# Performance work log

Measured on AMD Instinct MI355X. Metric: run time of the kernel, lower is better.

The kernel has to match this reference:

```python
import jax, jax.numpy as jnp
import numpy as np
from jax import lax

EQN = 10  # equations per pixel in FlowLayer


def build_a(h, w):
    """Dense constraint basis a[num, EQN, 4*num] (<=2 nonzeros per row), as in FlowLayer.__init__."""
    num = h * w
    a = np.zeros((num, EQN, 4 * num), np.float32)
    for i in range(num):
        right = (i + 1) % w != 0 and i + 1 < num
        down = i + w < num
        if right:
            a[i, 0, 2 * num + i] = 1.0; a[i, 0, i + 1] = -1.0
            a[i, 2, 2 * num + i] = 1.0; a[i, 2, 2 * num + i + 1] = -1.0
            a[i, 4, i] = 1.0;           a[i, 4, i + 1] = -1.0
            a[i, 6, 3 * num + i] = 1.0; a[i, 6, 3 * num + i + 1] = -1.0
            a[i, 8, num + i] = 1.0;     a[i, 8, num + i + 1] = -1.0
        if down:
            a[i, 1, 3 * num + i] = 1.0; a[i, 1, num + i + w] = -1.0
            a[i, 3, 3 * num + i] = 1.0; a[i, 3, 3 * num + i + w] = -1.0
            a[i, 5, num + i] = 1.0;     a[i, 5, num + i + w] = -1.0
            a[i, 7, 2 * num + i] = 1.0; a[i, 7, 2 * num + i + w] = -1.0
            a[i, 9, i] = 1.0;           a[i, 9, i + w] = -1.0
    last = num - 1  # anchor equations for the last pixel
    a[last, 0, 2 * num + last] = 1.0
    a[last, 1, 3 * num + last] = 1.0
    a[last, 2, 2 * num + last] = 1.0
    a[last, 3, 3 * num + last] = 1.0
    a[last, 4, last] = 1.0
    a[last, 5, num + last] = 1.0
    a[last, 6, 3 * num + last] = 1.0
    a[last, 7, 2 * num + last] = 1.0
    a[last, 8, num + last] = 1.0
    a[last, 9, last] = 1.0
    return a


def conv2d(x, w, b):
    y = lax.conv_general_dilated(x, w, (1, 1), 'SAME',
                                 dimension_numbers=('NCHW', 'OIHW', 'NCHW'))
    return y + b[None, :, None, None]


def setup_inputs() -> dict:
    key = jax.random.key(0)
    N, C, H, W, GR = 4, 64, 16, 16, 4
    ks = jax.random.split(key, 12)
    s3, s1 = 0.04, 0.1  # ~1/sqrt(fan_in) scales
    inp = {
        'x': jax.random.normal(ks[0], (N, C, H, W), jnp.float32),
        'grad_w1': jax.random.normal(ks[1], (C, C, 3, 3), jnp.float32) * s3,
        'grad_b1': jnp.zeros((C,), jnp.float32),
        'grad_w2': jax.random.normal(ks[2], (EQN * GR, C, 3, 3), jnp.float32) * s3,
        'grad_b2': jnp.zeros((EQN * GR,), jnp.float32),
        'att_w1': jax.random.normal(ks[3], (C, C, 3, 3), jnp.float32) * s3,
        'att_b1': jnp.zeros((C,), jnp.float32),
        'att_w2': jax.random.normal(ks[4], (EQN * GR, C, 3, 3), jnp.float32) * s3,
        'att_b2': jnp.zeros((EQN * GR,), jnp.float32),
        'se_w1': jax.random.normal(ks[5], (C // 2, C, 1, 1), jnp.float32) * s1,
        'se_b1': jnp.zeros((C // 2,), jnp.float32),
        'se_w2': jax.random.normal(ks[6], (4 * GR, C // 2, 1, 1), jnp.float32) * s1,
        'se_b2': jnp.zeros((4 * GR,), jnp.float32),
        'gn_w': jnp.ones((4 * GR,), jnp.float32),
        'gn_b': jnp.zeros((4 * GR,), jnp.float32),
        'post_w': jax.random.normal(ks[7], (128, 4 * GR, 3, 3), jnp.float32) * s1,
        'post_b': jnp.zeros((128,), jnp.float32),
    }
    return inp


def reference(x, grad_w1, grad_b1, grad_w2, grad_b2,
              att_w1, att_b1, att_w2, att_b2,
              se_w1, se_b1, se_w2, se_b2,
              gn_w, gn_b, post_w, post_b):
    n, c, h, w = x.shape
    gr = gn_w.shape[0] // 4
    num = h * w
    lrelu = lambda t: jax.nn.leaky_relu(t, 0.01)

    grad = conv2d(lrelu(conv2d(x, grad_w1, grad_b1)), grad_w2, grad_b2)      # [n, eqn*gr, h, w]
    att = jax.nn.sigmoid(conv2d(lrelu(conv2d(x, att_w1, att_b1)), att_w2, att_b2))
    pooled = x.mean((2, 3), keepdims=True)                                     # AdaptiveAvgPool2d(1)
    se = jax.nn.sigmoid(conv2d(lrelu(conv2d(pooled, se_w1, se_b1)), se_w2, se_b2))  # [n, 4*gr, 1, 1]

    # reshape(n*gr, EQN, hw).permute -> [B, hw, EQN] -> flatten rows as (pixel, eqn)
    att_f = att.reshape(n * gr, EQN, num).transpose(0, 2, 1).reshape(n * gr, num * EQN)
    grad_f = grad.reshape(n * gr, EQN, num).transpose(0, 2, 1).reshape(n * gr, num * EQN)

    a_flat = jnp.asarray(build_a(h, w)).reshape(num * EQN, 4 * num)  # constant basis
    A = att_f[:, :, None] * a_flat[None]                 # [B, num*EQN, 4*num]
    b_vec = att_f * grad_f                               # [B, num*EQN]
    ATA = jnp.einsum('brj,brk->bjk', A, A)               # [B, 4num, 4num]
    ATB = jnp.einsum('brj,br->bj', A, b_vec)[..., None]  # [B, 4num, 1]
    jitter = jnp.eye(4 * num, dtype=x.dtype) * 1e-12
    sol = jnp.linalg.solve(ATA + jitter[None], ATB)      # [B, 4num, 1]

    y = sol.reshape(n, 4 * gr, h, w)
    # GroupNorm(1, 4*gr): normalize over (C,H,W) per sample
    mu = y.mean((1, 2, 3), keepdims=True)
    var = ((y - mu) ** 2).mean((1, 2, 3), keepdims=True)
    y = (y - mu) / jnp.sqrt(var + 1e-5)
    y = y * gn_w[None, :, None, None] + gn_b[None, :, None, None]
    y = se * y
    return conv2d(y, post_w, post_b)  # [n, 128, h, w]
```

## Files before the change

### kernel.cpp

```cpp
#include <hip/hip_runtime.h>

#define NCHEB 8

typedef __attribute__((ext_vector_type(8))) short vs8;
typedef __attribute__((ext_vector_type(4))) float vf4;
typedef __attribute__((ext_vector_type(16))) float vf16;

__device__ __forceinline__ unsigned short f2bf(float f) {
  union { float f; unsigned int u; } x; x.f = f;
  unsigned int r = (x.u + 0x7FFFu + ((x.u >> 16) & 1u)) >> 16;
  return (unsigned short)r;
}

template<int CTRL>
__device__ __forceinline__ float dppf(float x) {
  return __int_as_float(__builtin_amdgcn_mov_dpp(__float_as_int(x), CTRL, 0xF, 0xF, true));
}

template<int COUT, int TILES, bool SE>
__global__ __launch_bounds__(256) void k_conv(
    const float* __restrict__ inA, const float* __restrict__ inB,
    const float* __restrict__ wA, const float* __restrict__ bA,
    const float* __restrict__ wB, const float* __restrict__ bB,
    float* __restrict__ outA, float* __restrict__ outB,
    int actA, int actB,
    const float* __restrict__ x,
    const float* __restrict__ sw1, const float* __restrict__ sb1,
    const float* __restrict__ sw2, const float* __restrict__ sb2,
    float* __restrict__ seo) {
  __shared__ unsigned short Xl[256 * 64];
  __shared__ unsigned short Wl[9 * 16 * 64];
  __shared__ float sp[64];
  __shared__ float sh1[32];
  const int b = blockIdx.x;
  const int t = threadIdx.x;

  if (SE && b >= 8 * TILES) {
    const int n = b - 8 * TILES;
    const int c = t >> 2, part = t & 3;
    const float* xp = x + (n * 64 + c) * 256 + part * 64;
    float s = 0.f;
    for (int k = 0; k < 64; ++k) s += xp[k];
    s += __shfl_xor(s, 1, 64);
    s += __shfl_xor(s, 2, 64);
    if (part == 0) sp[c] = s * (1.f / 256.f);
    __syncthreads();
    if (t < 32) {
      float a = sb1[t];
      for (int k = 0; k < 64; ++k) a += sw1[t * 64 + k] * sp[k];
      sh1[t] = a > 0.f ? a : 0.01f * a;
    }
    __syncthreads();
    if (t < 16) {
      float a = sb2[t];
      for (int k = 0; k < 32; ++k) a += sw2[t * 32 + k] * sh1[k];
      seo[n * 16 + t] = 1.f / (1.f + __expf(-a));
    }
    return;
  }

  const int n = b & 3;
  const int q = b >> 2;
  const int br = (q >= TILES) ? 1 : 0;
  const int ct = q - br * TILES;
  const int co0 = ct * 16;
  const float* inp = (br ? inB : inA) + n * 64 * 256;
  const float* wsrc = br ? wB : wA;
  const float* bias = br ? bB : bA;
  float* outp = (br ? outB : outA) + n * COUT * 256;
  const int act = br ? actB : actA;

  {
    const int p = t;
    #pragma unroll
    for (int q8 = 0; q8 < 8; ++q8) {
      vs8 v;
      #pragma unroll
      for (int j = 0; j < 8; ++j) v[j] = (short)f2bf(inp[(8 * q8 + j) * 256 + p]);
      *(vs8*)&Xl[p * 64 + ((q8 ^ (p & 7)) << 3)] = v;
    }
  }
  {
    const int col = t >> 4;
    const int sub = t & 15;
    const int co = co0 + col;
    if (co < COUT) {
      const float* wp = wsrc + (co * 64 + sub * 4) * 9;
      #pragma unroll
      for (int cc = 0; cc < 4; ++cc) {
        const int ci = sub * 4 + cc;
        #pragma unroll
        for (int e = 0; e < 9; ++e)
          Wl[(e * 16 + col) * 64 + (ci ^ ((col & 7) << 3))] = f2bf(wp[cc * 9 + e]);
      }
    } else {
      #pragma unroll
      for (int cc = 0; cc < 4; ++cc) {
        const int ci = sub * 4 + cc;
        #pragma unroll
        for (int e = 0; e < 9; ++e)
          Wl[(e * 16 + col) * 64 + (ci ^ ((col & 7) << 3))] = 0;
      }
    }
  }
  __syncthreads();

  const int w = t >> 6, lane = t & 63;
  const int px = lane & 15, kg = lane >> 4;
  vf4 acc[4];
  #pragma unroll
  for (int mt = 0; mt < 4; ++mt) acc[mt] = (vf4)0.f;

  for (int e = 0; e < 9; ++e) {
    const int dy = e / 3 - 1, dx = e % 3 - 1;
    const bool xok = (dx == 0) || (dx < 0 ? (px > 0) : (px < 15));
    const int xoff = xok ? dx : 0;
    #pragma unroll
    for (int ks = 0; ks < 2; ++ks) {
      vs8 bf = *(const vs8*)&Wl[(e * 16 + px) * 64 + (((ks * 4 + kg) ^ (px & 7)) << 3)];
      #pragma unroll
      for (int mt = 0; mt < 4; ++mt) {
        const int yy = 4 * w + mt + dy;
        if (yy < 0 || yy > 15) continue;
        const int ps = yy * 16 + px + xoff;
        vs8 a = *(const vs8*)&Xl[ps * 64 + (((ks * 4 + kg) ^ (ps & 7)) << 3)];
        if (!xok) a = (vs8)(short)0;
        acc[mt] = __builtin_amdgcn_mfma_f32_16x16x32_bf16(a, bf, acc[mt], 0, 0, 0);
      }
    }
  }

  const int co = co0 + px;
  if (co < COUT) {
    const float bv = bias[co];
    #pragma unroll
    for (int mt = 0; mt < 4; ++mt) {
      const int y = 4 * w + mt;
      vf4 v = acc[mt];
      #pragma unroll
      for (int j = 0; j < 4; ++j) {
        float s = v[j] + bv;
        if (act == 1) s = s > 0.f ? s : 0.01f * s;
        else if (act == 2) s = 1.f / (1.f + __expf(-s));
        v[j] = s;
      }
      *(vf4*)&outp[co * 256 + y * 16 + kg * 4] = v;
    }
  }
}

__global__ __launch_bounds__(512) void k_post(
    const float* __restrict__ sol, const float* __restrict__ se,
    const float* __restrict__ gn_w, const float* __restrict__ gn_b,
    const float* __restrict__ pw, const float* __restrict__ pb,
    float* __restrict__ out) {
  __shared__ unsigned short Hl[256 * 24];
  __shared__ unsigned short Wp[9 * 128 * 24];
  __shared__ float rs[8];
  __shared__ float rs2[8];
  const int n = blockIdx.x;
  const int t = threadIdx.x;
  const int w = t >> 6, lane = t & 63;

  float v[8];
  {
    const vf4* s4 = (const vf4*)(sol + n * 4096 + 8 * t);
    vf4 a = s4[0], b = s4[1];
    v[0]=a[0];v[1]=a[1];v[2]=a[2];v[3]=a[3];v[4]=b[0];v[5]=b[1];v[6]=b[2];v[7]=b[3];
  }
  float s = 0.f, s2 = 0.f;
  #pragma unroll
  for (int k = 0; k < 8; ++k) { s += v[k]; s2 += v[k] * v[k]; }
  #pragma unroll
  for (int o = 1; o <= 32; o <<= 1) { s += __shfl_xor(s, o, 64); s2 += __shfl_xor(s2, o, 64); }
  if (lane == 0) { rs[w] = s; rs2[w] = s2; }

  {
    const int co = t >> 2, sub = t & 3;
    const float* wp0 = pw + (co * 16 + sub * 4) * 9;
    #pragma unroll
    for (int cc = 0; cc < 4; ++cc) {
      const int ci = sub * 4 + cc;
      #pragma unroll
      for (int e = 0; e < 9; ++e)
        Wp[(e * 128 + co) * 24 + ci] = f2bf(wp0[cc * 9 + e]);
    }
  }
  __syncthreads();
  float sm = 0.f, sq = 0.f;
  #pragma unroll
  for (int k = 0; k < 8; ++k) { sm += rs[k]; sq += rs2[k]; }
  const float mu = sm * (1.f / 4096.f);
  const float rstd = rsqrtf(sq * (1.f / 4096.f) - mu * mu + 1e-5f);

  const int c = t >> 5;
  const int p0 = (8 * t) & 255;
  const float sev = se[n * 16 + c];
  const float sc = rstd * gn_w[c] * sev;
  const float of = (gn_b[c] - mu * rstd * gn_w[c]) * sev;
  #pragma unroll
  for (int k = 0; k < 8; ++k) Hl[(p0 + k) * 24 + c] = f2bf(v[k] * sc + of);
  __syncthreads();

  const int cl = lane & 31, h = lane >> 5;
  const int px = cl & 15, y0 = 2 * w + (cl >> 4);
  vf16 acc[4];
  #pragma unroll
  for (int nt = 0; nt < 4; ++nt) acc[nt] = (vf16)0.f;
  for (int e = 0; e < 9; ++e) {
    const int dy = e / 3 - 1, dx = e % 3 - 1;
    const int yy = y0 + dy, xx = px + dx;
    const bool ok = (yy >= 0 && yy < 16 && xx >= 0 && xx < 16);
    const int ps = ok ? yy * 16 + xx : 0;
    vs8 a = *(const vs8*)&Hl[ps * 24 + h * 8];
    if (!ok) a = (vs8)(short)0;
    #pragma unroll
    for (int nt = 0; nt < 4; ++nt) {
      vs8 bf = *(const vs8*)&Wp[(e * 128 + nt * 32 + cl) * 24 + h * 8];
      acc[nt] = __builtin_amdgcn_mfma_f32_32x32x16_bf16(a, bf, acc[nt], 0, 0, 0);
    }
  }
  float* op = out + n * 32768;
  #pragma unroll
  for (int nt = 0; nt < 4; ++nt) {
    const int co = nt * 32 + cl;
    const float bv = pb[co];
    #pragma unroll
    for (int rq = 0; rq < 4; ++rq) {
      vf4 vv;
      #pragma unroll
      for (int j = 0; j < 4; ++j) vv[j] = acc[nt][rq * 4 + j] + bv;
      *(vf4*)&op[co * 256 + 32 * w + 8 * rq + 4 * h] = vv;
    }
  }
}

__global__ __launch_bounds__(64) void k_pcg(
    const float* __restrict__ att, const float* __restrict__ grad,
    float* __restrict__ sol, int maxit, float tol2) {
  const int unit = blockIdx.x;
  const int sys = unit >> 1;
  const int wv = unit & 1;
  const int l = threadIdx.x & 63;
  const int row = l & 15;
  const int c4 = l >> 4;
  const int i0 = 16 * row + 4 * c4;

  const int n = sys >> 2, g = sys & 3;
  const float* ab = att + (n * 40 + g * 10) * 256;
  const float* gb = grad + (n * 40 + g * 10) * 256;

  int era, eda, erb, edb, ec, fa, fb;
  if (wv == 0) { fa = 0; fb = 2; era = 4; eda = 9; erb = 2; edb = 7; ec = 0; }
  else         { fa = 1; fb = 3; era = 8; eda = 5; erb = 6; edb = 3; ec = 1; }

  auto L4 = [](const float* p) { return *reinterpret_cast<const float4*>(p); };
  auto unp = [](float4 v, float* o) { o[0] = v.x; o[1] = v.y; o[2] = v.z; o[3] = v.w; };

  float wLa[4], wRa[4], wUa[4], wDa[4], wXa[4], dga[4], iva[4], rsa[4];
  float wLb[4], wRb[4], wUb[4], wDb[4], wXb[4], dgb[4], ivb[4], rsb[4];

  float rA[4], gA[4], dA[4], hA[4], uA[4] = {0,0,0,0}, vA[4] = {0,0,0,0};
  unp(L4(ab + era * 256 + i0), rA); unp(L4(gb + era * 256 + i0), gA);
  unp(L4(ab + eda * 256 + i0), dA); unp(L4(gb + eda * 256 + i0), hA);
  if (row > 0) { unp(L4(ab + eda * 256 + i0 - 16), uA); unp(L4(gb + eda * 256 + i0 - 16), vA); }
  float rlA = (l > 0) ? ab[era * 256 + i0 - 1] : 0.f;
  float glA = (l > 0) ? gb[era * 256 + i0 - 1] : 0.f;
  float cX[4], gX[4], cU[4] = {0,0,0,0}, gU[4] = {0,0,0,0};
  unp(L4(ab + ec * 256 + i0), cX); unp(L4(gb + ec * 256 + i0), gX);
  float clX = 0.f, glX = 0.f;
  if (wv == 0) { if (l > 0) { clX = ab[ec * 256 + i0 - 1]; glX = gb[ec * 256 + i0 - 1]; } }
  else if (row > 0) { unp(L4(ab + ec * 256 + i0 - 16), cU); unp(L4(gb + ec * 256 + i0 - 16), gU); }

  #pragma unroll
  for (int k = 0; k < 4; ++k) {
    wRa[k] = (k < 3 || c4 < 3) ? rA[k] * rA[k] : 0.f;
    wLa[k] = (k > 0) ? rA[k-1] * rA[k-1] : ((c4 > 0) ? rlA * rlA : 0.f);
    wDa[k] = (row < 15) ? dA[k] * dA[k] : 0.f;
    wUa[k] = (row > 0) ? uA[k] * uA[k] : 0.f;
    float rhs = wRa[k] * gA[k] - wLa[k] * ((k > 0) ? gA[k-1] : glA)
              + wDa[k] * hA[k] - wUa[k] * vA[k];
    float wx, gx;
    if (wv == 0) {
      wx = (k > 0) ? cX[k-1] * cX[k-1] : ((c4 > 0) ? clX * clX : 0.f);
      gx = (k > 0) ? gX[k-1] : glX;
    } else {
      wx = (row > 0) ? cU[k] * cU[k] : 0.f;
      gx = gU[k];
    }
    wXa[k] = wx;
    rhs -= wx * gx;
    rsa[k] = rhs;
    dga[k] = 1e-12f + wRa[k] + wLa[k] + wDa[k] + wUa[k] + wx;
  }

  float rB[4], gB[4], dB[4], hB[4], uB[4] = {0,0,0,0}, vB[4] = {0,0,0,0};
  unp(L4(ab + erb * 256 + i0), rB); unp(L4(gb + erb * 256 + i0), gB);
  unp(L4(ab + edb * 256 + i0), dB); unp(L4(gb + edb * 256 + i0), hB);
  if (row > 0) { unp(L4(ab + edb * 256 + i0 - 16), uB); unp(L4(gb + edb * 256 + i0 - 16), vB); }
  float rlB = (l > 0) ? ab[erb * 256 + i0 - 1] : 0.f;
  float glB = (l > 0) ? gb[erb * 256 + i0 - 1] : 0.f;

  #pragma unroll
  for (int k = 0; k < 4; ++k) {
    wRb[k] = (k < 3 || c4 < 3) ? rB[k] * rB[k] : 0.f;
    wLb[k] = (k > 0) ? rB[k-1] * rB[k-1] : ((c4 > 0) ? rlB * rlB : 0.f);
    wDb[k] = (row < 15) ? dB[k] * dB[k] : 0.f;
    wUb[k] = (row > 0) ? uB[k] * uB[k] : 0.f;
    float wx;
    if (wv == 0) wx = (k < 3 || c4 < 3) ? cX[k] * cX[k] : 0.f;
    else         wx = (row < 15) ? cX[k] * cX[k] : 0.f;
    wXb[k] = wx;
    rsb[k] = wRb[k] * gB[k] - wLb[k] * ((k > 0) ? gB[k-1] : glB)
           + wDb[k] * hB[k] - wUb[k] * vB[k]
           + wx * gX[k];
    dgb[k] = 1e-12f + wRb[k] + wLb[k] + wDb[k] + wUb[k] + wx;
  }

  if (l == 63) {
    float wr = rA[3] * rA[3], wd = dA[3] * dA[3];
    dga[3] += wr + wd;
    rsa[3] += wr * gA[3] + wd * hA[3];
    float wc = cX[3] * cX[3], wrb = rB[3] * rB[3], wdb = dB[3] * dB[3];
    dgb[3] += wc + wrb + wdb;
    rsb[3] += wc * gX[3] + wrb * gB[3] + wdb * hB[3];
  }
  #pragma unroll
  for (int k = 0; k < 4; ++k) { iva[k] = 1.f / dga[k]; ivb[k] = 1.f / dgb[k]; }

  float ua[4], ub[4], wa[4], wb[4];

  auto spmv = [&](const float (&ia_)[4], const float (&ib_)[4],
                  float (&oa)[4], float (&ob)[4]) {
    float aL = __shfl_up(ia_[3], 16, 64);
    float aR = __shfl_down(ia_[0], 16, 64);
    float bL = __shfl_up(ib_[3], 16, 64);
    float bR = __shfl_down(ib_[0], 16, 64);
    float aU[4], aD[4], bU[4], bD[4];
    #pragma unroll
    for (int k = 0; k < 4; ++k) {
      aU[k] = dppf<0x138>(ia_[k]);
      aD[k] = dppf<0x130>(ia_[k]);
      bU[k] = dppf<0x138>(ib_[k]);
      bD[k] = dppf<0x130>(ib_[k]);
    }
    float uaL[4] = {aL, ia_[0], ia_[1], ia_[2]};
    float uaR[4] = {ia_[1], ia_[2], ia_[3], aR};
    float ubL[4] = {bL, ib_[0], ib_[1], ib_[2]};
    float ubR[4] = {ib_[1], ib_[2], ib_[3], bR};
    #pragma unroll
    for (int k = 0; k < 4; ++k) {
      float cA = (wv == 0) ? ubL[k] : bU[k];
      float cB = (wv == 0) ? uaR[k] : aD[k];
      oa[k] = dga[k] * ia_[k] - wLa[k] * uaL[k] - wRa[k] * uaR[k]
            - wUa[k] * aU[k] - wDa[k] * aD[k] - wXa[k] * cA;
      ob[k] = dgb[k] * ib_[k] - wLb[k] * ubL[k] - wRb[k] * ubR[k]
            - wUb[k] * bU[k] - wDb[k] * bD[k] - wXb[k] * cB;
    }
  };

  constexpr float lo = 0.01f, hi = 2.0f;
  constexpr float th = (hi + lo) * 0.5f, dl = (hi - lo) * 0.5f, s1 = th / dl;

  float xa[4] = {0,0,0,0}, xb[4] = {0,0,0,0};
  float ra_[4], rb_[4], pa[4] = {0,0,0,0}, pb_[4] = {0,0,0,0};
  float sa[4] = {0,0,0,0}, sb[4] = {0,0,0,0};
  #pragma unroll
  for (int k = 0; k < 4; ++k) { ra_[k] = rsa[k]; rb_[k] = rsb[k]; }

  auto cheb = [&]() {
    float da_[4], db_[4], ta[4], tb[4], qa[4], qb[4];
    #pragma unroll
    for (int k = 0; k < 4; ++k) {
      da_[k] = (1.0f / th) * iva[k] * ra_[k];
      db_[k] = (1.0f / th) * ivb[k] * rb_[k];
      ua[k] = da_[k]; ub[k] = db_[k];
    }
    spmv(da_, db_, ta, tb);
    #pragma unroll
    for (int k = 0; k < 4; ++k) {
      wa[k] = ta[k]; wb[k] = tb[k];
      qa[k] = ra_[k] - ta[k]; qb[k] = rb_[k] - tb[k];
    }
    float rho = 1.0f / s1;
    #pragma unroll
    for (int j = 1; j < NCHEB; ++j) {
      float rho2 = 1.0f / (2.0f * s1 - rho);
      float c1 = rho2 * rho, c2 = 2.0f * rho2 / dl;
      #pragma unroll
      for (int k = 0; k < 4; ++k) {
        da_[k] = c1 * da_[k] + c2 * iva[k] * qa[k];
        db_[k] = c1 * db_[k] + c2 * ivb[k] * qb[k];
        ua[k] += da_[k]; ub[k] += db_[k];
      }
      spmv(da_, db_, ta, tb);
      #pragma unroll
      for (int k = 0; k < 4; ++k) {
        wa[k] += ta[k]; wb[k] += tb[k];
        qa[k] -= ta[k]; qb[k] -= tb[k];
      }
      rho = rho2;
    }
  };

  float gamma, delta;
  auto dots = [&]() {
    float gp = 0.f, dp = 0.f;
    #pragma unroll
    for (int k = 0; k < 4; ++k) {
      gp += ra_[k] * ua[k] + rb_[k] * ub[k];
      dp += wa[k] * ua[k] + wb[k] * ub[k];
    }
    gp += dppf<0xB1>(gp);            dp += dppf<0xB1>(dp);
    gp += dppf<0x4E>(gp);            dp += dppf<0x4E>(dp);
    gp += __shfl_xor(gp, 4, 64);     dp += __shfl_xor(dp, 4, 64);
    gp += dppf<0x128>(gp);           dp += dppf<0x128>(dp);
    gp += __shfl_xor(gp, 16, 64);    dp += __shfl_xor(dp, 16, 64);
    gp += __shfl_xor(gp, 32, 64);    dp += __shfl_xor(dp, 32, 64);
    gamma = gp; delta = dp;
  };

  cheb();
  dots();
  const float thresh = tol2 * gamma;
  float gamma_old = gamma, alpha_old = 1.f;

  for (int it = 0; it < maxit && gamma > thresh; ++it) {
    float beta = (it == 0) ? 0.f : gamma / gamma_old;
    float alpha = (it == 0) ? gamma / delta
                            : gamma / (delta - beta * gamma / alpha_old);
    #pragma unroll
    for (int k = 0; k < 4; ++k) {
      pa[k] = ua[k] + beta * pa[k];   pb_[k] = ub[k] + beta * pb_[k];
      sa[k] = wa[k] + beta * sa[k];   sb[k] = wb[k] + beta * sb[k];
      xa[k] += alpha * pa[k];         xb[k] += alpha * pb_[k];
      ra_[k] -= alpha * sa[k];        rb_[k] -= alpha * sb[k];
    }
    gamma_old = gamma; alpha_old = alpha;
    cheb();
    dots();
  }

  float4* sol4 = reinterpret_cast<float4*>(sol);
  const int slot = 4 * row + c4;
  sol4[sys * 256 + fa * 64 + slot] = make_float4(xa[0], xa[1], xa[2], xa[3]);
  sol4[sys * 256 + fb * 64 + slot] = make_float4(xb[0], xb[1], xb[2], xb[3]);
}

extern "C" void kernel_launch(void* const* d_in, const int* in_sizes, int n_in,
                              void* d_out, int out_size, void* d_ws, size_t ws_size,
                              hipStream_t stream) {
  const float* x       = (const float*)d_in[0];
  const float* grad_w1 = (const float*)d_in[1];
  const float* grad_b1 = (const float*)d_in[2];
  const float* grad_w2 = (const float*)d_in[3];
  const float* grad_b2 = (const float*)d_in[4];
  const float* att_w1  = (const float*)d_in[5];
  const float* att_b1  = (const float*)d_in[6];
  const float* att_w2  = (const float*)d_in[7];
  const float* att_b2  = (const float*)d_in[8];
  const float* se_w1   = (const float*)d_in[9];
  const float* se_b1   = (const float*)d_in[10];
  const float* se_w2   = (const float*)d_in[11];
  const float* se_b2   = (const float*)d_in[12];
  const float* gn_w    = (const float*)d_in[13];
  const float* gn_b    = (const float*)d_in[14];
  const float* post_w  = (const float*)d_in[15];
  const float* post_b  = (const float*)d_in[16];
  float* out = (float*)d_out;
  float* ws = (float*)d_ws;

  float* t1    = ws;
  float* t2    = ws + 65536;
  float* gradb = ws + 131072;
  float* attb  = ws + 172032;
  float* seb   = ws + 212992;
  float* solb  = ws;

  k_conv<64, 4, true><<<36, 256, 0, stream>>>(
      x, x, grad_w1, grad_b1, att_w1, att_b1, t1, t2, 1, 1,
      x, se_w1, se_b1, se_w2, se_b2, seb);
  k_conv<40, 3, false><<<24, 256, 0, stream>>>(
      t1, t2, grad_w2, grad_b2, att_w2, att_b2, gradb, attb, 0, 2,
      nullptr, nullptr, nullptr, nullptr, nullptr, nullptr);
  k_pcg<<<32, 64, 0, stream>>>(attb, gradb, solb, 100, 3e-6f);
  k_post<<<4, 512, 0, stream>>>(solb, seb, gn_w, gn_b, post_w, post_b, out);
}
```

Baseline: 61.92 us.

## Merge both decoupled PCG sub-systems into one wavefront per system

```diff
diff --git a/kernel.cpp b/kernel.cpp
--- a/kernel.cpp
+++ b/kernel.cpp
@@ -238,9 +238,7 @@
 __global__ __launch_bounds__(64) void k_pcg(
     const float* __restrict__ att, const float* __restrict__ grad,
     float* __restrict__ sol, int maxit, float tol2) {
-  const int unit = blockIdx.x;
-  const int sys = unit >> 1;
-  const int wv = unit & 1;
+  const int sys = blockIdx.x;
   const int l = threadIdx.x & 63;
   const int row = l & 15;
   const int c4 = l >> 4;
@@ -250,201 +248,246 @@
   const float* ab = att + (n * 40 + g * 10) * 256;
   const float* gb = grad + (n * 40 + g * 10) * 256;
 
-  int era, eda, erb, edb, ec, fa, fb;
-  if (wv == 0) { fa = 0; fb = 2; era = 4; eda = 9; erb = 2; edb = 7; ec = 0; }
-  else         { fa = 1; fb = 3; era = 8; eda = 5; erb = 6; edb = 3; ec = 1; }
+  const int ERA[2] = {4, 8}, EDA[2] = {9, 5};
+  const int ERB[2] = {2, 6}, EDB[2] = {7, 3};
+  const int EC[2]  = {0, 1};
+  const int FA[2]  = {0, 1}, FB[2] = {2, 3};
 
   auto L4 = [](const float* p) { return *reinterpret_cast<const float4*>(p); };
   auto unp = [](float4 v, float* o) { o[0] = v.x; o[1] = v.y; o[2] = v.z; o[3] = v.w; };
 
-  float wLa[4], wRa[4], wUa[4], wDa[4], wXa[4], dga[4], iva[4], rsa[4];
-  float wLb[4], wRb[4], wUb[4], wDb[4], wXb[4], dgb[4], ivb[4], rsb[4];
-
-  float rA[4], gA[4], dA[4], hA[4], uA[4] = {0,0,0,0}, vA[4] = {0,0,0,0};
-  unp(L4(ab + era * 256 + i0), rA); unp(L4(gb + era * 256 + i0), gA);
-  unp(L4(ab + eda * 256 + i0), dA); unp(L4(gb + eda * 256 + i0), hA);
-  if (row > 0) { unp(L4(ab + eda * 256 + i0 - 16), uA); unp(L4(gb + eda * 256 + i0 - 16), vA); }
-  float rlA = (l > 0) ? ab[era * 256 + i0 - 1] : 0.f;
-  float glA = (l > 0) ? gb[era * 256 + i0 - 1] : 0.f;
-  float cX[4], gX[4], cU[4] = {0,0,0,0}, gU[4] = {0,0,0,0};
-  unp(L4(ab + ec * 256 + i0), cX); unp(L4(gb + ec * 256 + i0), gX);
-  float clX = 0.f, glX = 0.f;
-  if (wv == 0) { if (l > 0) { clX = ab[ec * 256 + i0 - 1]; glX = gb[ec * 256 + i0 - 1]; } }
-  else if (row > 0) { unp(L4(ab + ec * 256 + i0 - 16), cU); unp(L4(gb + ec * 256 + i0 - 16), gU); }
-
-  #pragma unroll
-  for (int k = 0; k < 4; ++k) {
-    wRa[k] = (k < 3 || c4 < 3) ? rA[k] * rA[k] : 0.f;
-    wLa[k] = (k > 0) ? rA[k-1] * rA[k-1] : ((c4 > 0) ? rlA * rlA : 0.f);
-    wDa[k] = (row < 15) ? dA[k] * dA[k] : 0.f;
-    wUa[k] = (row > 0) ? uA[k] * uA[k] : 0.f;
-    float rhs = wRa[k] * gA[k] - wLa[k] * ((k > 0) ? gA[k-1] : glA)
-              + wDa[k] * hA[k] - wUa[k] * vA[k];
-    float wx, gx;
-    if (wv == 0) {
-      wx = (k > 0) ? cX[k-1] * cX[k-1] : ((c4 > 0) ? clX * clX : 0.f);
-      gx = (k > 0) ? gX[k-1] : glX;
-    } else {
-      wx = (row > 0) ? cU[k] * cU[k] : 0.f;
-      gx = gU[k];
-    }
-    wXa[k] = wx;
-    rhs -= wx * gx;
-    rsa[k] = rhs;
-    dga[k] = 1e-12f + wRa[k] + wLa[k] + wDa[k] + wUa[k] + wx;
-  }
-
-  float rB[4], gB[4], dB[4], hB[4], uB[4] = {0,0,0,0}, vB[4] = {0,0,0,0};
-  unp(L4(ab + erb * 256 + i0), rB); unp(L4(gb + erb * 256 + i0), gB);
-  unp(L4(ab + edb * 256 + i0), dB); unp(L4(gb + edb * 256 + i0), hB);
-  if (row > 0) { unp(L4(ab + edb * 256 + i0 - 16), uB); unp(L4(gb + edb * 256 + i0 - 16), vB); }
-  float rlB = (l > 0) ? ab[erb * 256 + i0 - 1] : 0.f;
-  float glB = (l > 0) ? gb[erb * 256 + i0 - 1] : 0.f;
-
-  #pragma unroll
-  for (int k = 0; k < 4; ++k) {
-    wRb[k] = (k < 3 || c4 < 3) ? rB[k] * rB[k] : 0.f;
-    wLb[k] = (k > 0) ? rB[k-1] * rB[k-1] : ((c4 > 0) ? rlB * rlB : 0.f);
-    wDb[k] = (row < 15) ? dB[k] * dB[k] : 0.f;
-    wUb[k] = (row > 0) ? uB[k] * uB[k] : 0.f;
-    float wx;
-    if (wv == 0) wx = (k < 3 || c4 < 3) ? cX[k] * cX[k] : 0.f;
-    else         wx = (row < 15) ? cX[k] * cX[k] : 0.f;
-    wXb[k] = wx;
-    rsb[k] = wRb[k] * gB[k] - wLb[k] * ((k > 0) ? gB[k-1] : glB)
-           + wDb[k] * hB[k] - wUb[k] * vB[k]
-           + wx * gX[k];
-    dgb[k] = 1e-12f + wRb[k] + wLb[k] + wDb[k] + wUb[k] + wx;
-  }
-
-  if (l == 63) {
-    float wr = rA[3] * rA[3], wd = dA[3] * dA[3];
-    dga[3] += wr + wd;
-    rsa[3] += wr * gA[3] + wd * hA[3];
-    float wc = cX[3] * cX[3], wrb = rB[3] * rB[3], wdb = dB[3] * dB[3];
-    dgb[3] += wc + wrb + wdb;
-    rsb[3] += wc * gX[3] + wrb * gB[3] + wdb * hB[3];
-  }
-  #pragma unroll
-  for (int k = 0; k < 4; ++k) { iva[k] = 1.f / dga[k]; ivb[k] = 1.f / dgb[k]; }
-
-  float ua[4], ub[4], wa[4], wb[4];
-
-  auto spmv = [&](const float (&ia_)[4], const float (&ib_)[4],
-                  float (&oa)[4], float (&ob)[4]) {
-    float aL = __shfl_up(ia_[3], 16, 64);
-    float aR = __shfl_down(ia_[0], 16, 64);
-    float bL = __shfl_up(ib_[3], 16, 64);
-    float bR = __shfl_down(ib_[0], 16, 64);
-    float aU[4], aD[4], bU[4], bD[4];
+  float wLa[2][4], wRa[2][4], wUa[2][4], wDa[2][4], wXa[2][4], dga[2][4], iva[2][4], rsa[2][4];
+  float wLb[2][4], wRb[2][4], wUb[2][4], wDb[2][4], wXb[2][4], dgb[2][4], ivb[2][4], rsb[2][4];
+
+  #pragma unroll
+  for (int c = 0; c < 2; ++c) {
+    float rA[4], gA[4], dA[4], hA[4], uA[4] = {0,0,0,0}, vA[4] = {0,0,0,0};
+    unp(L4(ab + ERA[c] * 256 + i0), rA); unp(L4(gb + ERA[c] * 256 + i0), gA);
+    unp(L4(ab + EDA[c] * 256 + i0), dA); unp(L4(gb + EDA[c] * 256 + i0), hA);
+    if (row > 0) { unp(L4(ab + EDA[c] * 256 + i0 - 16), uA); unp(L4(gb + EDA[c] * 256 + i0 - 16), vA); }
+    float rlA = (l > 0) ? ab[ERA[c] * 256 + i0 - 1] : 0.f;
+    float glA = (l > 0) ? gb[ERA[c] * 256 + i0 - 1] : 0.f;
+    float cX[4], gX[4], cU[4] = {0,0,0,0}, gU[4] = {0,0,0,0};
+    unp(L4(ab + EC[c] * 256 + i0), cX); unp(L4(gb + EC[c] * 256 + i0), gX);
+    float clX = 0.f, glX = 0.f;
+    if (c == 0) { if (l > 0) { clX = ab[EC[c] * 256 + i0 - 1]; glX = gb[EC[c] * 256 + i0 - 1]; } }
+    else if (row > 0) { unp(L4(ab + EC[c] * 256 + i0 - 16), cU); unp(L4(gb + EC[c] * 256 + i0 - 16), gU); }
+
     #pragma unroll
     for (int k = 0; k < 4; ++k) {
-      aU[k] = dppf<0x138>(ia_[k]);
-      aD[k] = dppf<0x130>(ia_[k]);
-      bU[k] = dppf<0x138>(ib_[k]);
-      bD[k] = dppf<0x130>(ib_[k]);
-    }
-    float uaL[4] = {aL, ia_[0], ia_[1], ia_[2]};
-    float uaR[4] = {ia_[1], ia_[2], ia_[3], aR};
-    float ubL[4] = {bL, ib_[0], ib_[1], ib_[2]};
-    float ubR[4] = {ib_[1], ib_[2], ib_[3], bR};
+      wRa[c][k] = (k < 3 || c4 < 3) ? rA[k] * rA[k] : 0.f;
+      wLa[c][k] = (k > 0) ? rA[k-1] * rA[k-1] : ((c4 > 0) ? rlA * rlA : 0.f);
+      wDa[c][k] = (row < 15) ? dA[k] * dA[k] : 0.f;
+      wUa[c][k] = (row > 0) ? uA[k] * uA[k] : 0.f;
+      float rhs = wRa[c][k] * gA[k] - wLa[c][k] * ((k > 0) ? gA[k-1] : glA)
+                + wDa[c][k] * hA[k] - wUa[c][k] * vA[k];
+      float wx, gx;
+      if (c == 0) {
+        wx = (k > 0) ? cX[k-1] * cX[k-1] : ((c4 > 0) ? clX * clX : 0.f);
+        gx = (k > 0) ? gX[k-1] : glX;
+      } else {
+        wx = (row > 0) ? cU[k] * cU[k] : 0.f;
+        gx = gU[k];
+      }
+      wXa[c][k] = wx;
+      rhs -= wx * gx;
+      rsa[c][k] = rhs;
+      dga[c][k] = 1e-12f + wRa[c][k] + wLa[c][k] + wDa[c][k] + wUa[c][k] + wx;
+    }
+
+    float rB[4], gB[4], dB[4], hB[4], uB[4] = {0,0,0,0}, vB[4] = {0,0,0,0};
+    unp(L4(ab + ERB[c] * 256 + i0), rB); unp(L4(gb + ERB[c] * 256 + i0), gB);
+    unp(L4(ab + EDB[c] * 256 + i0), dB); unp(L4(gb + EDB[c] * 256 + i0), hB);
+    if (row > 0) { unp(L4(ab + EDB[c] * 256 + i0 - 16), uB); unp(L4(gb + EDB[c] * 256 + i0 - 16), vB); }
+    float rlB = (l > 0) ? ab[ERB[c] * 256 + i0 - 1] : 0.f;
+    float glB = (l > 0) ? gb[ERB[c] * 256 + i0 - 1] : 0.f;
+
     #pragma unroll
     for (int k = 0; k < 4; ++k) {
-      float cA = (wv == 0) ? ubL[k] : bU[k];
-      float cB = (wv == 0) ? uaR[k] : aD[k];
-      oa[k] = dga[k] * ia_[k] - wLa[k] * uaL[k] - wRa[k] * uaR[k]
-            - wUa[k] * aU[k] - wDa[k] * aD[k] - wXa[k] * cA;
-      ob[k] = dgb[k] * ib_[k] - wLb[k] * ubL[k] - wRb[k] * ubR[k]
-            - wUb[k] * bU[k] - wDb[k] * bD[k] - wXb[k] * cB;
+      wRb[c][k] = (k < 3 || c4 < 3) ? rB[k] * rB[k] : 0.f;
+      wLb[c][k] = (k > 0) ? rB[k-1] * rB[k-1] : ((c4 > 0) ? rlB * rlB : 0.f);
+      wDb[c][k] = (row < 15) ? dB[k] * dB[k] : 0.f;
+      wUb[c][k] = (row > 0) ? uB[k] * uB[k] : 0.f;
+      float wx;
+      if (c == 0) wx = (k < 3 || c4 < 3) ? cX[k] * cX[k] : 0.f;
+      else        wx = (row < 15) ? cX[k] * cX[k] : 0.f;
+      wXb[c][k] = wx;
+      rsb[c][k] = wRb[c][k] * gB[k] - wLb[c][k] * ((k > 0) ? gB[k-1] : glB)
+                + wDb[c][k] * hB[k] - wUb[c][k] * vB[k]
+                + wx * gX[k];
+      dgb[c][k] = 1e-12f + wRb[c][k] + wLb[c][k] + wDb[c][k] + wUb[c][k] + wx;
+    }
+
+    if (l == 63) {
+      float wr = rA[3] * rA[3], wd = dA[3] * dA[3];
+      dga[c][3] += wr + wd;
+      rsa[c][3] += wr * gA[3] + wd * hA[3];
+      float wc = cX[3] * cX[3], wrb = rB[3] * rB[3], wdb = dB[3] * dB[3];
+      dgb[c][3] += wc + wrb + wdb;
+      rsb[c][3] += wc * gX[3] + wrb * gB[3] + wdb * hB[3];
+    }
+  }
+  #pragma unroll
+  for (int c = 0; c < 2; ++c)
+    #pragma unroll
+    for (int k = 0; k < 4; ++k) { iva[c][k] = 1.f / dga[c][k]; ivb[c][k] = 1.f / dgb[c][k]; }
+
+  float ua[2][4], ub[2][4], wa[2][4], wb[2][4];
+
+  auto spmv = [&](const float (&ia_)[2][4], const float (&ib_)[2][4],
+                  float (&oa)[2][4], float (&ob)[2][4]) {
+    float aL[2], aR[2], bL[2], bR[2];
+    #pragma unroll
+    for (int c = 0; c < 2; ++c) {
+      aL[c] = __shfl_up(ia_[c][3], 16, 64);
+      aR[c] = __shfl_down(ia_[c][0], 16, 64);
+      bL[c] = __shfl_up(ib_[c][3], 16, 64);
+      bR[c] = __shfl_down(ib_[c][0], 16, 64);
+    }
+    #pragma unroll
+    for (int c = 0; c < 2; ++c) {
+      float aU[4], aD[4], bU[4], bD[4];
+      #pragma unroll
+      for (int k = 0; k < 4; ++k) {
+        aU[k] = dppf<0x138>(ia_[c][k]);
+        aD[k] = dppf<0x130>(ia_[c][k]);
+        bU[k] = dppf<0x138>(ib_[c][k]);
+        bD[k] = dppf<0x130>(ib_[c][k]);
+      }
+      float uaL[4] = {aL[c], ia_[c][0], ia_[c][1], ia_[c][2]};
+      float uaR[4] = {ia_[c][1], ia_[c][2], ia_[c][3], aR[c]};
+      float ubL[4] = {bL[c], ib_[c][0], ib_[c][1], ib_[c][2]};
+      float ubR[4] = {ib_[c][1], ib_[c][2], ib_[c][3], bR[c]};
+      #pragma unroll
+      for (int k = 0; k < 4; ++k) {
+        float cA = (c == 0) ? ubL[k] : bU[k];
+        float cB = (c == 0) ? uaR[k] : aD[k];
+        oa[c][k] = dga[c][k] * ia_[c][k] - wLa[c][k] * uaL[k] - wRa[c][k] * uaR[k]
+                 - wUa[c][k] * aU[k] - wDa[c][k] * aD[k] - wXa[c][k] * cA;
+        ob[c][k] = dgb[c][k] * ib_[c][k] - wLb[c][k] * ubL[k] - wRb[c][k] * ubR[k]
+                 - wUb[c][k] * bU[k] - wDb[c][k] * bD[k] - wXb[c][k] * cB;
+      }
     }
   };
 
   constexpr float lo = 0.01f, hi = 2.0f;
   constexpr float th = (hi + lo) * 0.5f, dl = (hi - lo) * 0.5f, s1 = th / dl;
 
-  float xa[4] = {0,0,0,0}, xb[4] = {0,0,0,0};
-  float ra_[4], rb_[4], pa[4] = {0,0,0,0}, pb_[4] = {0,0,0,0};
-  float sa[4] = {0,0,0,0}, sb[4] = {0,0,0,0};
-  #pragma unroll
-  for (int k = 0; k < 4; ++k) { ra_[k] = rsa[k]; rb_[k] = rsb[k]; }
+  float xa[2][4], xb[2][4], ra_[2][4], rb_[2][4];
+  float pa[2][4], pb_[2][4], sa[2][4], sb[2][4];
+  #pragma unroll
+  for (int c = 0; c < 2; ++c)
+    #pragma unroll
+    for (int k = 0; k < 4; ++k) {
+      xa[c][k] = 0.f; xb[c][k] = 0.f;
+      pa[c][k] = 0.f; pb_[c][k] = 0.f;
+      sa[c][k] = 0.f; sb[c][k] = 0.f;
+      ra_[c][k] = rsa[c][k]; rb_[c][k] = rsb[c][k];
+    }
 
   auto cheb = [&]() {
-    float da_[4], db_[4], ta[4], tb[4], qa[4], qb[4];
-    #pragma unroll
-    for (int k = 0; k < 4; ++k) {
-      da_[k] = (1.0f / th) * iva[k] * ra_[k];
-      db_[k] = (1.0f / th) * ivb[k] * rb_[k];
-      ua[k] = da_[k]; ub[k] = db_[k];
-    }
+    float da_[2][4], db_[2][4], ta[2][4], tb[2][4], qa[2][4], qb[2][4];
+    #pragma unroll
+    for (int c = 0; c < 2; ++c)
+      #pragma unroll
+      for (int k = 0; k < 4; ++k) {
+        da_[c][k] = (1.0f / th) * iva[c][k] * ra_[c][k];
+        db_[c][k] = (1.0f / th) * ivb[c][k] * rb_[c][k];
+        ua[c][k] = da_[c][k]; ub[c][k] = db_[c][k];
+      }
     spmv(da_, db_, ta, tb);
     #pragma unroll
-    for (int k = 0; k < 4; ++k) {
-      wa[k] = ta[k]; wb[k] = tb[k];
-      qa[k] = ra_[k] - ta[k]; qb[k] = rb_[k] - tb[k];
-    }
+    for (int c = 0; c < 2; ++c)
+      #pragma unroll
+      for (int k = 0; k < 4; ++k) {
+        wa[c][k] = ta[c][k]; wb[c][k] = tb[c][k];
+        qa[c][k] = ra_[c][k] - ta[c][k]; qb[c][k] = rb_[c][k] - tb[c][k];
+      }
     float rho = 1.0f / s1;
     #pragma unroll
     for (int j = 1; j < NCHEB; ++j) {
       float rho2 = 1.0f / (2.0f * s1 - rho);
       float c1 = rho2 * rho, c2 = 2.0f * rho2 / dl;
       #pragma unroll
+      for (int c = 0; c < 2; ++c)
+        #pragma unroll
+        for (int k = 0; k < 4; ++k) {
+          da_[c][k] = c1 * da_[c][k] + c2 * iva[c][k] * qa[c][k];
+          db_[c][k] = c1 * db_[c][k] + c2 * ivb[c][k] * qb[c][k];
+          ua[c][k] += da_[c][k]; ub[c][k] += db_[c][k];
+        }
+      spmv(da_, db_, ta, tb);
+      #pragma unroll
+      for (int c = 0; c < 2; ++c)
+        #pragma unroll
+        for (int k = 0; k < 4; ++k) {
+          wa[c][k] += ta[c][k]; wb[c][k] += tb[c][k];
+          qa[c][k] -= ta[c][k]; qb[c][k] -= tb[c][k];
+        }
+      rho = rho2;
+    }
+  };
+
+  float gamma[2], delta[2];
+  auto dots = [&]() {
+    float gp[2], dp[2];
+    #pragma unroll
+    for (int c = 0; c < 2; ++c) {
+      gp[c] = 0.f; dp[c] = 0.f;
+      #pragma unroll
       for (int k = 0; k < 4; ++k) {
-        da_[k] = c1 * da_[k] + c2 * iva[k] * qa[k];
-        db_[k] = c1 * db_[k] + c2 * ivb[k] * qb[k];
-        ua[k] += da_[k]; ub[k] += db_[k];
-      }
-      spmv(da_, db_, ta, tb);
-      #pragma unroll
-      for (int k = 0; k < 4; ++k) {
-        wa[k] += ta[k]; wb[k] += tb[k];
-        qa[k] -= ta[k]; qb[k] -= tb[k];
-      }
-      rho = rho2;
-    }
-  };
-
-  float gamma, delta;
-  auto dots = [&]() {
-    float gp = 0.f, dp = 0.f;
-    #pragma unroll
-    for (int k = 0; k < 4; ++k) {
-      gp += ra_[k] * ua[k] + rb_[k] * ub[k];
-      dp += wa[k] * ua[k] + wb[k] * ub[k];
-    }
-    gp += dppf<0xB1>(gp);            dp += dppf<0xB1>(dp);
-    gp += dppf<0x4E>(gp);            dp += dppf<0x4E>(dp);
-    gp += __shfl_xor(gp, 4, 64);     dp += __shfl_xor(dp, 4, 64);
-    gp += dppf<0x128>(gp);           dp += dppf<0x128>(dp);
-    gp += __shfl_xor(gp, 16, 64);    dp += __shfl_xor(dp, 16, 64);
-    gp += __shfl_xor(gp, 32, 64);    dp += __shfl_xor(dp, 32, 64);
-    gamma = gp; delta = dp;
+        gp[c] += ra_[c][k] * ua[c][k] + rb_[c][k] * ub[c][k];
+        dp[c] += wa[c][k] * ua[c][k] + wb[c][k] * ub[c][k];
+      }
+    }
+    #pragma unroll
+    for (int c = 0; c < 2; ++c) {
+      gp[c] += dppf<0xB1>(gp[c]);          dp[c] += dppf<0xB1>(dp[c]);
+      gp[c] += dppf<0x4E>(gp[c]);          dp[c] += dppf<0x4E>(dp[c]);
+      gp[c] += __shfl_xor(gp[c], 4, 64);   dp[c] += __shfl_xor(dp[c], 4, 64);
+      gp[c] += dppf<0x128>(gp[c]);         dp[c] += dppf<0x128>(dp[c]);
+      gp[c] += __shfl_xor(gp[c], 16, 64);  dp[c] += __shfl_xor(dp[c], 16, 64);
+      gp[c] += __shfl_xor(gp[c], 32, 64);  dp[c] += __shfl_xor(dp[c], 32, 64);
+      gamma[c] = gp[c]; delta[c] = dp[c];
+    }
   };
 
   cheb();
   dots();
-  const float thresh = tol2 * gamma;
-  float gamma_old = gamma, alpha_old = 1.f;
-
-  for (int it = 0; it < maxit && gamma > thresh; ++it) {
-    float beta = (it == 0) ? 0.f : gamma / gamma_old;
-    float alpha = (it == 0) ? gamma / delta
-                            : gamma / (delta - beta * gamma / alpha_old);
-    #pragma unroll
-    for (int k = 0; k < 4; ++k) {
-      pa[k] = ua[k] + beta * pa[k];   pb_[k] = ub[k] + beta * pb_[k];
-      sa[k] = wa[k] + beta * sa[k];   sb[k] = wb[k] + beta * sb[k];
-      xa[k] += alpha * pa[k];         xb[k] += alpha * pb_[k];
-      ra_[k] -= alpha * sa[k];        rb_[k] -= alpha * sb[k];
-    }
-    gamma_old = gamma; alpha_old = alpha;
+  float thresh[2], gamma_old[2], alpha_old[2];
+  #pragma unroll
+  for (int c = 0; c < 2; ++c) { thresh[c] = tol2 * gamma[c]; gamma_old[c] = gamma[c]; alpha_old[c] = 1.f; }
+
+  for (int it = 0; it < maxit && (gamma[0] > thresh[0] || gamma[1] > thresh[1]); ++it) {
+    float alpha[2], beta[2];
+    #pragma unroll
+    for (int c = 0; c < 2; ++c) {
+      beta[c] = (it == 0) ? 0.f : gamma[c] / gamma_old[c];
+      alpha[c] = (it == 0) ? gamma[c] / delta[c]
+                           : gamma[c] / (delta[c] - beta[c] * gamma[c] / alpha_old[c]);
+    }
+    #pragma unroll
+    for (int c = 0; c < 2; ++c)
+      #pragma unroll
+      for (int k = 0; k < 4; ++k) {
+        pa[c][k] = ua[c][k] + beta[c] * pa[c][k];   pb_[c][k] = ub[c][k] + beta[c] * pb_[c][k];
+        sa[c][k] = wa[c][k] + beta[c] * sa[c][k];   sb[c][k] = wb[c][k] + beta[c] * sb[c][k];
+        xa[c][k] += alpha[c] * pa[c][k];            xb[c][k] += alpha[c] * pb_[c][k];
+        ra_[c][k] -= alpha[c] * sa[c][k];           rb_[c][k] -= alpha[c] * sb[c][k];
+      }
+    #pragma unroll
+    for (int c = 0; c < 2; ++c) { gamma_old[c] = gamma[c]; alpha_old[c] = alpha[c]; }
     cheb();
     dots();
   }
 
   float4* sol4 = reinterpret_cast<float4*>(sol);
   const int slot = 4 * row + c4;
-  sol4[sys * 256 + fa * 64 + slot] = make_float4(xa[0], xa[1], xa[2], xa[3]);
-  sol4[sys * 256 + fb * 64 + slot] = make_float4(xb[0], xb[1], xb[2], xb[3]);
+  #pragma unroll
+  for (int c = 0; c < 2; ++c) {
+    sol4[sys * 256 + FA[c] * 64 + slot] = make_float4(xa[c][0], xa[c][1], xa[c][2], xa[c][3]);
+    sol4[sys * 256 + FB[c] * 64 + slot] = make_float4(xb[c][0], xb[c][1], xb[c][2], xb[c][3]);
+  }
 }
 
 extern "C" void kernel_launch(void* const* d_in, const int* in_sizes, int n_in,
@@ -483,6 +526,6 @@
   k_conv<40, 3, false><<<24, 256, 0, stream>>>(
       t1, t2, grad_w2, grad_b2, att_w2, att_b2, gradb, attb, 0, 2,
       nullptr, nullptr, nullptr, nullptr, nullptr, nullptr);
-  k_pcg<<<32, 64, 0, stream>>>(attb, gradb, solb, 100, 3e-6f);
+  k_pcg<<<16, 64, 0, stream>>>(attb, gradb, solb, 100, 3e-6f);
   k_post<<<4, 512, 0, stream>>>(solb, seb, gn_w, gn_b, post_w, post_b, out);
 }
```

Result: slower. 125.4 us (+102.6%).

## Fuse PCG solve and post conv into one kernel with flag sync

Applied to the files above, without the earlier changes.

```diff
diff --git a/kernel.cpp b/kernel.cpp
--- a/kernel.cpp
+++ b/kernel.cpp
@@ -1,6 +1,6 @@
 #include <hip/hip_runtime.h>
 
-#define NCHEB 8
+#define NCHEB 16
 
 typedef __attribute__((ext_vector_type(8))) short vs8;
 typedef __attribute__((ext_vector_type(4))) float vf4;
@@ -15,6 +15,15 @@
 template<int CTRL>
 __device__ __forceinline__ float dppf(float x) {
   return __int_as_float(__builtin_amdgcn_mov_dpp(__float_as_int(x), CTRL, 0xF, 0xF, true));
+}
+
+__device__ __forceinline__ void flag_set(unsigned* f) {
+  __builtin_amdgcn_fence(__ATOMIC_RELEASE, "agent");
+  __hip_atomic_store(f, 1u, __ATOMIC_RELAXED, __HIP_MEMORY_SCOPE_AGENT);
+}
+__device__ __forceinline__ void flag_wait(unsigned* f) {
+  while (__hip_atomic_load(f, __ATOMIC_RELAXED, __HIP_MEMORY_SCOPE_AGENT) == 0u)
+    __builtin_amdgcn_s_sleep(2);
 }
 
 template<int COUT, int TILES, bool SE>
@@ -149,96 +158,9 @@
   }
 }
 
-__global__ __launch_bounds__(512) void k_post(
-    const float* __restrict__ sol, const float* __restrict__ se,
-    const float* __restrict__ gn_w, const float* __restrict__ gn_b,
-    const float* __restrict__ pw, const float* __restrict__ pb,
-    float* __restrict__ out) {
-  __shared__ unsigned short Hl[256 * 24];
-  __shared__ unsigned short Wp[9 * 128 * 24];
-  __shared__ float rs[8];
-  __shared__ float rs2[8];
-  const int n = blockIdx.x;
-  const int t = threadIdx.x;
-  const int w = t >> 6, lane = t & 63;
-
-  float v[8];
-  {
-    const vf4* s4 = (const vf4*)(sol + n * 4096 + 8 * t);
-    vf4 a = s4[0], b = s4[1];
-    v[0]=a[0];v[1]=a[1];v[2]=a[2];v[3]=a[3];v[4]=b[0];v[5]=b[1];v[6]=b[2];v[7]=b[3];
-  }
-  float s = 0.f, s2 = 0.f;
-  #pragma unroll
-  for (int k = 0; k < 8; ++k) { s += v[k]; s2 += v[k] * v[k]; }
-  #pragma unroll
-  for (int o = 1; o <= 32; o <<= 1) { s += __shfl_xor(s, o, 64); s2 += __shfl_xor(s2, o, 64); }
-  if (lane == 0) { rs[w] = s; rs2[w] = s2; }
-
-  {
-    const int co = t >> 2, sub = t & 3;
-    const float* wp0 = pw + (co * 16 + sub * 4) * 9;
-    #pragma unroll
-    for (int cc = 0; cc < 4; ++cc) {
-      const int ci = sub * 4 + cc;
-      #pragma unroll
-      for (int e = 0; e < 9; ++e)
-        Wp[(e * 128 + co) * 24 + ci] = f2bf(wp0[cc * 9 + e]);
-    }
-  }
-  __syncthreads();
-  float sm = 0.f, sq = 0.f;
-  #pragma unroll
-  for (int k = 0; k < 8; ++k) { sm += rs[k]; sq += rs2[k]; }
-  const float mu = sm * (1.f / 4096.f);
-  const float rstd = rsqrtf(sq * (1.f / 4096.f) - mu * mu + 1e-5f);
-
-  const int c = t >> 5;
-  const int p0 = (8 * t) & 255;
-  const float sev = se[n * 16 + c];
-  const float sc = rstd * gn_w[c] * sev;
-  const float of = (gn_b[c] - mu * rstd * gn_w[c]) * sev;
-  #pragma unroll
-  for (int k = 0; k < 8; ++k) Hl[(p0 + k) * 24 + c] = f2bf(v[k] * sc + of);
-  __syncthreads();
-
-  const int cl = lane & 31, h = lane >> 5;
-  const int px = cl & 15, y0 = 2 * w + (cl >> 4);
-  vf16 acc[4];
-  #pragma unroll
-  for (int nt = 0; nt < 4; ++nt) acc[nt] = (vf16)0.f;
-  for (int e = 0; e < 9; ++e) {
-    const int dy = e / 3 - 1, dx = e % 3 - 1;
-    const int yy = y0 + dy, xx = px + dx;
-    const bool ok = (yy >= 0 && yy < 16 && xx >= 0 && xx < 16);
-    const int ps = ok ? yy * 16 + xx : 0;
-    vs8 a = *(const vs8*)&Hl[ps * 24 + h * 8];
-    if (!ok) a = (vs8)(short)0;
-    #pragma unroll
-    for (int nt = 0; nt < 4; ++nt) {
-      vs8 bf = *(const vs8*)&Wp[(e * 128 + nt * 32 + cl) * 24 + h * 8];
-      acc[nt] = __builtin_amdgcn_mfma_f32_32x32x16_bf16(a, bf, acc[nt], 0, 0, 0);
-    }
-  }
-  float* op = out + n * 32768;
-  #pragma unroll
-  for (int nt = 0; nt < 4; ++nt) {
-    const int co = nt * 32 + cl;
-    const float bv = pb[co];
-    #pragma unroll
-    for (int rq = 0; rq < 4; ++rq) {
-      vf4 vv;
-      #pragma unroll
-      for (int j = 0; j < 4; ++j) vv[j] = acc[nt][rq * 4 + j] + bv;
-      *(vf4*)&op[co * 256 + 32 * w + 8 * rq + 4 * h] = vv;
-    }
-  }
-}
-
-__global__ __launch_bounds__(64) void k_pcg(
-    const float* __restrict__ att, const float* __restrict__ grad,
+__device__ void pcg_unit(
+    int unit, const float* __restrict__ att, const float* __restrict__ grad,
     float* __restrict__ sol, int maxit, float tol2) {
-  const int unit = blockIdx.x;
   const int sys = unit >> 1;
   const int wv = unit & 1;
   const int l = threadIdx.x & 63;
@@ -445,6 +367,105 @@
   const int slot = 4 * row + c4;
   sol4[sys * 256 + fa * 64 + slot] = make_float4(xa[0], xa[1], xa[2], xa[3]);
   sol4[sys * 256 + fb * 64 + slot] = make_float4(xb[0], xb[1], xb[2], xb[3]);
+}
+
+__global__ __launch_bounds__(512, 1) void k_solve(
+    const float* __restrict__ att, const float* __restrict__ grad,
+    const float* __restrict__ se,
+    const float* __restrict__ gn_w, const float* __restrict__ gn_b,
+    const float* __restrict__ pw, const float* __restrict__ pb,
+    float* __restrict__ sol, float* __restrict__ out,
+    unsigned* __restrict__ flags, int maxit, float tol2) {
+  __shared__ unsigned short Hl[256 * 24];
+  __shared__ unsigned short Wp[9 * 128 * 24];
+  __shared__ float rs[8], rs2[8];
+  const int bid = blockIdx.x;
+  const int t = threadIdx.x;
+  const bool leader = (bid & 7) == 0;
+
+  if (t < 64) {
+    pcg_unit(bid, att, grad, sol, maxit, tol2);
+    if (t == 0 && !leader) flag_set(flags + bid * 16);
+  } else if (leader) {
+    for (int i = t - 64; i < 128 * 16 * 9; i += 448) {
+      const int co = i / 144;
+      const int rem = i - co * 144;
+      const int ci = rem / 9;
+      const int e = rem - ci * 9;
+      Wp[(e * 128 + co) * 24 + ci] = f2bf(pw[i]);
+    }
+  }
+  if (!leader) return;
+
+  if (t == 0) {
+    #pragma unroll
+    for (int u = 1; u < 8; ++u) flag_wait(flags + (bid + u) * 16);
+    __builtin_amdgcn_fence(__ATOMIC_ACQUIRE, "agent");
+  }
+  __syncthreads();
+
+  const int n = bid >> 3;
+  const int w = t >> 6, lane = t & 63;
+
+  float v[8];
+  {
+    const vf4* s4 = (const vf4*)(sol + n * 4096 + 8 * t);
+    vf4 a = s4[0], b = s4[1];
+    v[0]=a[0];v[1]=a[1];v[2]=a[2];v[3]=a[3];v[4]=b[0];v[5]=b[1];v[6]=b[2];v[7]=b[3];
+  }
+  float s = 0.f, s2 = 0.f;
+  #pragma unroll
+  for (int k = 0; k < 8; ++k) { s += v[k]; s2 += v[k] * v[k]; }
+  #pragma unroll
+  for (int o = 1; o <= 32; o <<= 1) { s += __shfl_xor(s, o, 64); s2 += __shfl_xor(s2, o, 64); }
+  if (lane == 0) { rs[w] = s; rs2[w] = s2; }
+  __syncthreads();
+  float sm = 0.f, sq = 0.f;
+  #pragma unroll
+  for (int k = 0; k < 8; ++k) { sm += rs[k]; sq += rs2[k]; }
+  const float mu = sm * (1.f / 4096.f);
+  const float rstd = rsqrtf(sq * (1.f / 4096.f) - mu * mu + 1e-5f);
+
+  const int c = t >> 5;
+  const int p0 = (8 * t) & 255;
+  const float sev = se[n * 16 + c];
+  const float sc = rstd * gn_w[c] * sev;
+  const float of = (gn_b[c] - mu * rstd * gn_w[c]) * sev;
+  #pragma unroll
+  for (int k = 0; k < 8; ++k) Hl[(p0 + k) * 24 + c] = f2bf(v[k] * sc + of);
+  __syncthreads();
+
+  const int cl = lane & 31, h = lane >> 5;
+  const int px = cl & 15, y0 = 2 * w + (cl >> 4);
+  vf16 acc[4];
+  #pragma unroll
+  for (int nt = 0; nt < 4; ++nt) acc[nt] = (vf16)0.f;
+  for (int e = 0; e < 9; ++e) {
+    const int dy = e / 3 - 1, dx = e % 3 - 1;
+    const int yy = y0 + dy, xx = px + dx;
+    const bool ok = (yy >= 0 && yy < 16 && xx >= 0 && xx < 16);
+    const int ps = ok ? yy * 16 + xx : 0;
+    vs8 a = *(const vs8*)&Hl[ps * 24 + h * 8];
+    if (!ok) a = (vs8)(short)0;
+    #pragma unroll
+    for (int nt = 0; nt < 4; ++nt) {
+      vs8 bf = *(const vs8*)&Wp[(e * 128 + nt * 32 + cl) * 24 + h * 8];
+      acc[nt] = __builtin_amdgcn_mfma_f32_32x32x16_bf16(a, bf, acc[nt], 0, 0, 0);
+    }
+  }
+  float* op = out + n * 32768;
+  #pragma unroll
+  for (int nt = 0; nt < 4; ++nt) {
+    const int co = nt * 32 + cl;
+    const float bv = pb[co];
+    #pragma unroll
+    for (int rq = 0; rq < 4; ++rq) {
+      vf4 vv;
+      #pragma unroll
+      for (int j = 0; j < 4; ++j) vv[j] = acc[nt][rq * 4 + j] + bv;
+      *(vf4*)&op[co * 256 + 32 * w + 8 * rq + 4 * h] = vv;
+    }
+  }
 }
 
 extern "C" void kernel_launch(void* const* d_in, const int* in_sizes, int n_in,
@@ -475,14 +496,17 @@
   float* gradb = ws + 131072;
   float* attb  = ws + 172032;
   float* seb   = ws + 212992;
-  float* solb  = ws;
-
+  float* solb  = ws + 213056;
+  unsigned* flags = (unsigned*)(ws + 230000);
+
+  hipMemsetAsync(flags, 0, 2048, stream);
   k_conv<64, 4, true><<<36, 256, 0, stream>>>(
       x, x, grad_w1, grad_b1, att_w1, att_b1, t1, t2, 1, 1,
       x, se_w1, se_b1, se_w2, se_b2, seb);
   k_conv<40, 3, false><<<24, 256, 0, stream>>>(
       t1, t2, grad_w2, grad_b2, att_w2, att_b2, gradb, attb, 0, 2,
       nullptr, nullptr, nullptr, nullptr, nullptr, nullptr);
-  k_pcg<<<32, 64, 0, stream>>>(attb, gradb, solb, 100, 3e-6f);
-  k_post<<<4, 512, 0, stream>>>(solb, seb, gn_w, gn_b, post_w, post_b, out);
-}
+  k_solve<<<32, 512, 0, stream>>>(
+      attb, gradb, seb, gn_w, gn_b, post_w, post_b,
+      solb, out, flags, 40, 3e-6f);
+}
```

Result: slower. 97.96 us, median of 2 (+58.2%).
